# Performance work log

Hardware: AMD Instinct MI355X
Metric: run time of the kernel (lower is better)

The kernel has to match this reference:

```python
import jax, jax.numpy as jnp
import numpy as np
from jax import lax

DIM = 256
NUM_HEADS = 8
HEAD_DIM = DIM // NUM_HEADS  # 32
TOPK = 4
SCALE = 2  # spatial upscale factor between upper_feat grid and x grid


def conv1x1(x, W, b):
    # x: [B,Cin,H,W], W: [Cout,Cin], b: [Cout]
    return jnp.einsum('bchw,oc->bohw', x, W) + b[None, :, None, None]


def setup_inputs() -> dict:
    key = jax.random.key(0)
    ks = jax.random.split(key, 12)
    f32 = jnp.float32
    B, C, H, W = 2, DIM, 64, 64
    Hu, Wu = H // 2, W // 2
    s = 0.05
    return {
        'x': jax.random.normal(ks[0], (B, C, H, W), f32),
        'upper_feat': jax.random.normal(ks[1], (B, C, Hu, Wu), f32),
        # q: Conv(dim, all_head_dim, 1) with BN folded -> weight + bias
        'Wq': jax.random.normal(ks[2], (DIM, DIM), f32) * s,
        'bq': jnp.zeros((DIM,), f32),
        # kv: Conv(dim, 2*all_head_dim, 1)
        'Wkv': jax.random.normal(ks[3], (2 * DIM, DIM), f32) * s,
        'bkv': jnp.zeros((2 * DIM,), f32),
        # proj: Conv(all_head_dim, dim, 1)
        'Wproj': jax.random.normal(ks[4], (DIM, DIM), f32) * s,
        'bproj': jnp.zeros((DIM,), f32),
        # pe: depthwise 7x7 conv, groups=dim -> weight [dim,1,7,7]
        'Wpe': jax.random.normal(ks[5], (DIM, 1, 7, 7), f32) * s,
        'bpe': jnp.zeros((DIM,), f32),
        # gate_conv1d: Conv1d(2*head_dim, head_dim, 1) -> [head_dim, 2*head_dim]
        'Wg': jax.random.normal(ks[6], (HEAD_DIM, 2 * HEAD_DIM), f32) * s,
        'bg': jnp.zeros((HEAD_DIM,), f32),
    }


def reference(x, upper_feat, Wq, bq, Wkv, bkv, Wproj, bproj, Wpe, bpe, Wg, bg):
    B, C, H, W = x.shape
    N = H * W
    Hu, Wu = upper_feat.shape[2], upper_feat.shape[3]
    Nu = Hu * Wu
    nh, hd = NUM_HEADS, HEAD_DIM

    # queries from lower feature, keys/values from upper feature
    q = conv1x1(x, Wq, bq).reshape(B, nh, hd, N).transpose(0, 1, 3, 2)        # [B,h,N,hd]
    kv = conv1x1(upper_feat, Wkv, bkv).reshape(B, nh, 2 * hd, Nu).transpose(0, 1, 3, 2)
    k, v = kv[..., :hd], kv[..., hd:]                                         # [B,h,Nu,hd]

    sim = jnp.einsum('bhnd,bhmd->bhnm', q, k) * (hd ** -0.5)                  # [B,h,N,Nu]
    attn = jax.nn.softmax(sim, axis=-1)
    coarse_out = jnp.einsum('bhnm,bhmd->bhnd', attn, v)                       # [B,h,N,hd]

    # fine path: gumbel top-k selection over upper grid, gather 2x2 blocks from x grid
    f_kv = conv1x1(x, Wkv, bkv).reshape(B, nh, 2 * hd, N).transpose(0, 1, 3, 2)
    f_k, f_v = f_kv[..., :hd], f_kv[..., hd:]                                 # [B,h,N,hd]

    global_sim = sim.mean(axis=2)                                             # [B,h,Nu]
    gumbel = jax.random.gumbel(jax.random.key(42), global_sim.shape, global_sim.dtype)
    soft_weights = jax.nn.softmax(global_sim + gumbel, axis=-1)
    _, topk_idx = lax.top_k(soft_weights, TOPK)                               # [B,h,topk]

    h_idx = (topk_idx // Wu) * SCALE
    w_idx = (topk_idx % Wu) * SCALE
    idx = jnp.concatenate(
        [(h_idx + dh) * W + (w_idx + dw) for dh in range(SCALE) for dw in range(SCALE)],
        axis=-1,
    )                                                                          # [B,h,4*topk]

    topk_k = jnp.take_along_axis(f_k, idx[..., None], axis=2)                 # [B,h,4*topk,hd]
    topk_v = jnp.take_along_axis(f_v, idx[..., None], axis=2)

    fine_attn = jax.nn.softmax(jnp.einsum('bhnd,bhmd->bhnm', q, topk_k) * (hd ** -0.5), axis=-1)
    refined_out = jnp.einsum('bhnm,bhmd->bhnd', fine_attn, topk_v)            # [B,h,N,hd]

    fusion = jnp.concatenate([coarse_out, refined_out], axis=-1)              # [B,h,N,2hd]
    gate = jax.nn.sigmoid(jnp.einsum('bhnc,dc->bhnd', fusion, Wg) + bg)       # [B,h,N,hd]
    out = gate * refined_out + (1.0 - gate) * coarse_out

    out = out.transpose(0, 1, 3, 2).reshape(B, C, H, W)

    # positional encoding path: depthwise 7x7 conv on v, bilinear upsample
    v_r = v.transpose(0, 1, 3, 2).reshape(B, C, Hu, Wu)
    v_pe = lax.conv_general_dilated(
        v_r, Wpe, window_strides=(1, 1), padding=((3, 3), (3, 3)),
        dimension_numbers=('NCHW', 'OIHW', 'NCHW'), feature_group_count=C,
    ) + bpe[None, :, None, None]
    v_pe = jax.image.resize(v_pe, (B, C, H, W), method='bilinear')

    return conv1x1(out + v_pe, Wproj, bproj)
```

## Files before the change

### kernel.cpp

```cpp
#include <hip/hip_runtime.h>
#include <hip/hip_bf16.h>
#include <math.h>
#include <stdint.h>

#define NB   2
#define NC   256
#define NSP  4096
#define NUSP 1024
#define NHEADS 8
#define HDIM 32
constexpr float SCL  = 0.17677669529663687f;
constexpr float QSCL = 0.17677669529663687f * 1.4426950408889634f;

typedef short short8 __attribute__((ext_vector_type(8)));
typedef float f32x4  __attribute__((ext_vector_type(4)));

__device__ __forceinline__ float fexp2(float x) {
#if __has_builtin(__builtin_amdgcn_exp2f)
  return __builtin_amdgcn_exp2f(x);
#else
  return exp2f(x);
#endif
}

__device__ __align__(16) float g_kv    [NB * 512 * NUSP];
__device__ __align__(16) float g_qm    [NB * NHEADS * HDIM];
__device__ __align__(16) float g_vpe   [NB * NC * NSP];
__device__ __align__(16) short g_qbf   [NB * NHEADS * NSP * HDIM];
__device__ __align__(16) short g_kbf   [NB * NHEADS * NUSP * HDIM];
__device__ __align__(16) short g_vbf   [NB * NHEADS * HDIM * NUSP];
__device__ __align__(16) short g_tkKbf [NB * NHEADS * 16 * 32];
__device__ __align__(16) short g_tkVT  [NB * NHEADS * 32 * 32];
__device__ __align__(16) short g_xT    [NB * NSP * 256];
__device__ __align__(16) short g_uT    [NB * NUSP * 256];
__device__ __align__(16) short g_sumT  [NB * NSP * 256];
__device__ __align__(16) short g_wbf   [262144];
__device__ __align__(16) short g_wgbf  [2048];

__device__ __forceinline__ short f2bf(float f) {
  return (short)((__float_as_uint(f) + 0x8000u) >> 16);
}

__device__ __forceinline__ uint32_t pk2bf(float a, float b) {
  uint32_t lo = (__float_as_uint(a) + 0x8000u) >> 16;
  uint32_t hi = (__float_as_uint(b) + 0x8000u) & 0xffff0000u;
  return lo | hi;
}

__device__ __forceinline__ void threefry2x32_042(uint32_t x0, uint32_t x1,
                                                 uint32_t& r0, uint32_t& r1) {
  const uint32_t ks0 = 0u, ks1 = 42u, ks2 = 0u ^ 42u ^ 0x1BD11BDAu;
  x0 += ks0; x1 += ks1;
#define TFR(R) { x0 += x1; x1 = (x1 << (R)) | (x1 >> (32 - (R))); x1 ^= x0; }
  TFR(13) TFR(15) TFR(26) TFR(6)  x0 += ks1; x1 += ks2 + 1u;
  TFR(17) TFR(29) TFR(16) TFR(24) x0 += ks2; x1 += ks0 + 2u;
  TFR(13) TFR(15) TFR(26) TFR(6)  x0 += ks0; x1 += ks1 + 3u;
  TFR(17) TFR(29) TFR(16) TFR(24) x0 += ks1; x1 += ks2 + 4u;
  TFR(13) TFR(15) TFR(26) TFR(6)  x0 += ks2; x1 += ks0 + 5u;
#undef TFR
  r0 = x0; r1 = x1;
}

__device__ __forceinline__ float gumbel_at(uint32_t i) {
  uint32_t y0, y1;
  threefry2x32_042(0u, i, y0, y1);
  uint32_t bits = y0 ^ y1;
  uint32_t fb = (bits >> 9) | 0x3f800000u;
  float u = __uint_as_float(fb) - 1.0f;
  u = fmaxf(u, 1.17549435e-38f);
  return -logf(-logf(u));
}

__global__ __launch_bounds__(256) void k_pack_in(const float* __restrict__ x,
                                                 const float* __restrict__ upper,
                                                 const float* __restrict__ Wq,
                                                 const float* __restrict__ Wkv,
                                                 const float* __restrict__ Wproj,
                                                 const float* __restrict__ Wg) {
  const int sec = blockIdx.x;
  const int tid = threadIdx.x;
  if (sec < 160) {
    __shared__ float Ls[32][65];
    const float* src;
    short* dst;
    int b, n0, Nsp;
    if (sec < 128) { b = sec >> 6; n0 = (sec & 63) * 64; Nsp = NSP;
                     src = x + (size_t)b * 256 * NSP;  dst = g_xT + (size_t)b * NSP * 256; }
    else           { int s2 = sec - 128; b = s2 >> 4; n0 = (s2 & 15) * 64; Nsp = NUSP;
                     src = upper + (size_t)b * 256 * NUSP; dst = g_uT + (size_t)b * NUSP * 256; }
    for (int cc = 0; cc < 8; cc++) {
      __syncthreads();
      for (int i = tid; i < 2048; i += 256) {
        int d = i >> 6, nl = i & 63;
        Ls[d][nl] = src[(size_t)(cc * 32 + d) * Nsp + n0 + nl];
      }
      __syncthreads();
      int nl = tid >> 2, dseg = (tid & 3) * 8;
      short8 v;
      #pragma unroll
      for (int j = 0; j < 8; j++) v[j] = f2bf(Ls[dseg + j][nl]);
      *(short8*)&dst[(size_t)(n0 + nl) * 256 + cc * 32 + dseg] = v;
    }
  } else {
    if (sec == 160) {
      for (int i = tid; i < 512; i += 256) g_qm[i] = 0.f;
      #pragma unroll
      for (int j = 0; j < 8; j++) g_wgbf[tid * 8 + j] = f2bf(Wg[tid * 8 + j]);
    }
    int base = (sec - 160) * 8192 + tid * 32;
    const float* s;
    if (base < 65536)       s = Wq + base;
    else if (base < 196608) s = Wkv + (base - 65536);
    else                    s = Wproj + (base - 196608);
    short* d = g_wbf + base;
    #pragma unroll
    for (int j = 0; j < 8; j++) {
      float4 f = *(const float4*)&s[j * 4];
      d[j*4+0] = f2bf(f.x); d[j*4+1] = f2bf(f.y);
      d[j*4+2] = f2bf(f.z); d[j*4+3] = f2bf(f.w);
    }
  }
}

__device__ __forceinline__ void gemm_mfma(const short* __restrict__ Wbf,
                                          const short* __restrict__ ST,
                                          int b, int o0, int n0, int Nsp,
                                          int w, int col, int quad,
                                          f32x4 acc[4]) {
  const short* wrow = Wbf + (size_t)(o0 + w * 16 + col) * 256 + quad * 8;
  const short* srow = ST + ((size_t)b * Nsp + n0 + col) * 256 + quad * 8;
  #pragma unroll
  for (int kc = 0; kc < 8; kc++) {
    short8 af = *(const short8*)&wrow[kc * 32];
    #pragma unroll
    for (int t = 0; t < 4; t++) {
      short8 bf = *(const short8*)&srow[(size_t)(t * 16) * 256 + kc * 32];
      acc[t] = __builtin_amdgcn_mfma_f32_16x16x32_bf16(af, bf, acc[t], 0, 0, 0);
    }
  }
}

__global__ __launch_bounds__(256) void k_gemms(const float* __restrict__ bq,
                                               const float* __restrict__ bkv) {
  __shared__ float Ls[64][65];
  const int bx = blockIdx.x;
  const int tid = threadIdx.x;
  const int lane = tid & 63, w = tid >> 6, col = lane & 15, quad = lane >> 4;
  f32x4 acc[4] = {{0,0,0,0},{0,0,0,0},{0,0,0,0},{0,0,0,0}};

  if (bx < 512) {
    const int b = bx >> 8, o0 = ((bx >> 6) & 3) * 64, n0 = (bx & 63) * 64;
    gemm_mfma(g_wbf, g_xT, b, o0, n0, NSP, w, col, quad, acc);
    float sums[4];
    #pragma unroll
    for (int r = 0; r < 4; r++) {
      int ol = w * 16 + quad * 4 + r;
      float bv = bq[o0 + ol];
      float s = 0.f;
      #pragma unroll
      for (int t = 0; t < 4; t++) {
        float val = acc[t][r] + bv;
        Ls[ol][t * 16 + col] = val;
        s += val;
      }
      sums[r] = s;
    }
    #pragma unroll
    for (int st = 1; st < 16; st <<= 1)
      #pragma unroll
      for (int r = 0; r < 4; r++) sums[r] += __shfl_xor(sums[r], st, 64);
    if (col == 0) {
      #pragma unroll
      for (int r = 0; r < 4; r++)
        atomicAdd(&g_qm[b * 256 + o0 + w * 16 + quad * 4 + r], sums[r] * (1.0f / 4096.0f));
    }
    __syncthreads();
    int nl = tid >> 2, dseg = (tid & 3) * 8;
    #pragma unroll
    for (int hh = 0; hh < 2; hh++) {
      short8 v;
      #pragma unroll
      for (int j = 0; j < 8; j++) v[j] = f2bf(Ls[hh * 32 + dseg + j][nl] * QSCL);
      int bh = b * 8 + ((o0 + hh * 32) >> 5);
      *(short8*)&g_qbf[((size_t)bh * NSP + n0 + nl) * 32 + dseg] = v;
    }
  } else {
    const int idx = bx - 512;
    const int b = idx >> 7, o0 = ((idx >> 4) & 7) * 64, n0 = (idx & 15) * 64;
    gemm_mfma(g_wbf + 65536, g_uT, b, o0, n0, NUSP, w, col, quad, acc);
    #pragma unroll
    for (int r = 0; r < 4; r++) {
      int ol = w * 16 + quad * 4 + r;
      float bv = bkv[o0 + ol];
      float* orow = g_kv + ((size_t)b * 512 + o0 + ol) * NUSP + n0;
      #pragma unroll
      for (int t = 0; t < 4; t++) {
        float val = acc[t][r] + bv;
        orow[t * 16 + col] = val;
        Ls[ol][t * 16 + col] = val;
      }
    }
    __syncthreads();
    const int bh = b * 8 + (o0 >> 6);
    {
      int m = tid >> 2, dseg = (tid & 3) * 8;
      short8 v;
      #pragma unroll
      for (int j = 0; j < 8; j++) v[j] = f2bf(Ls[dseg + j][m]);
      *(short8*)&g_kbf[((size_t)bh * NUSP + n0 + m) * 32 + dseg] = v;
    }
    {
      int d = tid >> 3, m8 = (tid & 7) * 8;
      short8 v;
      #pragma unroll
      for (int j = 0; j < 8; j++) v[j] = f2bf(Ls[32 + d][m8 + j]);
      *(short8*)&g_vbf[((size_t)bh * 32 + d) * NUSP + n0 + m8] = v;
    }
  }
}

union MidSmem {
  struct {
    float zbuf[1024]; float qml[32]; float rv[256]; int ri[256];
    int chosen[4]; int pos[16]; float xg[16][256]; float wl[64][65];
  } t;
  struct {
    float src[32][33]; float pl[32][33]; float wk[49];
  } v;
};

__global__ __launch_bounds__(256) void k_mid(const float* __restrict__ x,
                                             const float* __restrict__ Wkv,
                                             const float* __restrict__ bkv,
                                             const float* __restrict__ Wpe,
                                             const float* __restrict__ bpe) {
  __shared__ MidSmem sm;
  const int tid = threadIdx.x;
  if (blockIdx.x < 16) {
    const int bh = blockIdx.x;
    const int b = bh >> 3, h = bh & 7;
    if (tid < 32) sm.t.qml[tid] = g_qm[bh * 32 + tid];
    __syncthreads();
    const float* kbase = g_kv + ((size_t)b * 512 + h * 64) * NUSP;
    float zv[4];
    #pragma unroll
    for (int r = 0; r < 4; r++) {
      int m = r * 256 + tid;
      float dot = 0.f;
      #pragma unroll 8
      for (int d = 0; d < 32; d++) dot += sm.t.qml[d] * kbase[(size_t)d * NUSP + m];
      float z = dot * SCL + gumbel_at((uint32_t)(bh * 1024 + m));
      zv[r] = z; sm.t.zbuf[m] = z;
    }
    __syncthreads();
    float mx = fmaxf(fmaxf(zv[0], zv[1]), fmaxf(zv[2], zv[3]));
    sm.t.rv[tid] = mx; __syncthreads();
    for (int st = 128; st > 0; st >>= 1) {
      if (tid < st) sm.t.rv[tid] = fmaxf(sm.t.rv[tid], sm.t.rv[tid + st]);
      __syncthreads();
    }
    float zmax = sm.t.rv[0]; __syncthreads();
    float sp = 0.f; float ev[4];
    #pragma unroll
    for (int r = 0; r < 4; r++) { ev[r] = __expf(zv[r] - zmax); sp += ev[r]; }
    sm.t.rv[tid] = sp; __syncthreads();
    for (int st = 128; st > 0; st >>= 1) {
      if (tid < st) sm.t.rv[tid] += sm.t.rv[tid + st];
      __syncthreads();
    }
    float ssum = sm.t.rv[0]; __syncthreads();
    #pragma unroll
    for (int r = 0; r < 4; r++) sm.t.zbuf[r * 256 + tid] = ev[r] / ssum;
    __syncthreads();
    for (int t = 0; t < 4; t++) {
      float bv = -2.0f; int bi = 0;
      #pragma unroll
      for (int r = 0; r < 4; r++) {
        int m = r * 256 + tid;
        float v = sm.t.zbuf[m];
        if (v > bv) { bv = v; bi = m; }
      }
      sm.t.rv[tid] = bv; sm.t.ri[tid] = bi; __syncthreads();
      for (int st = 128; st > 0; st >>= 1) {
        if (tid < st) {
          float v2 = sm.t.rv[tid + st]; int i2 = sm.t.ri[tid + st];
          if (v2 > sm.t.rv[tid] || (v2 == sm.t.rv[tid] && i2 < sm.t.ri[tid])) {
            sm.t.rv[tid] = v2; sm.t.ri[tid] = i2;
          }
        }
        __syncthreads();
      }
      if (tid == 0) { sm.t.chosen[t] = sm.t.ri[0]; sm.t.zbuf[sm.t.ri[0]] = -2.0f; }
      __syncthreads();
    }
    if (tid < 16) {
      int t = tid & 3, g2 = tid >> 2;
      int dh = g2 >> 1, dw = g2 & 1;
      int m = sm.t.chosen[t];
      int hi = (m >> 5) * 2 + dh, wi = (m & 31) * 2 + dw;
      sm.t.pos[g2 * 4 + t] = hi * 64 + wi;
    }
    __syncthreads();
    for (int i = tid; i < 16 * 256; i += 256) {
      int j = i >> 8, c = i & 255;
      sm.t.xg[j][c] = x[((size_t)b * 256 + c) * NSP + sm.t.pos[j]];
    }
    const int dd = tid & 63, jg = tid >> 6;
    const float bia = bkv[h * 64 + dd];
    float a4[4] = {bia, bia, bia, bia};
    for (int cc2 = 0; cc2 < 4; cc2++) {
      __syncthreads();
      for (int i = tid; i < 4096; i += 256) {
        int r = i >> 6, c = i & 63;
        sm.t.wl[r][c] = Wkv[(size_t)(h * 64 + r) * 256 + cc2 * 64 + c];
      }
      __syncthreads();
      #pragma unroll
      for (int jj = 0; jj < 4; jj++) {
        int j = jg * 4 + jj;
        float a = 0.f;
        #pragma unroll 8
        for (int c = 0; c < 64; c++) a += sm.t.xg[j][cc2 * 64 + c] * sm.t.wl[dd][c];
        a4[jj] += a;
      }
    }
    #pragma unroll
    for (int jj = 0; jj < 4; jj++) {
      int j = jg * 4 + jj;
      if (dd < 32) {
        g_tkKbf[((size_t)bh * 16 + j) * 32 + dd] = f2bf(a4[jj]);
      } else {
        int d = dd - 32;
        g_tkVT[((size_t)bh * 32 + d) * 32 + j] = f2bf(a4[jj]);
        g_tkVT[((size_t)bh * 32 + d) * 32 + 16 + j] = 0;
      }
    }
  } else {
    const int idx = blockIdx.x - 16;
    const int c = idx & 255, b = idx >> 8;
    const int h = c >> 5, d = c & 31;
    const float* vrow = g_kv + ((size_t)b * 512 + h * 64 + 32 + d) * NUSP;
    for (int i = tid; i < 1024; i += 256) sm.v.src[i >> 5][i & 31] = vrow[i];
    if (tid < 49) sm.v.wk[tid] = Wpe[c * 49 + tid];
    __syncthreads();
    const float bia = bpe[c];
    for (int i = tid; i < 1024; i += 256) {
      int hu = i >> 5, wu = i & 31;
      float s = bia;
      #pragma unroll
      for (int kh = 0; kh < 7; kh++) {
        int ih = hu + kh - 3;
        if (ih < 0 || ih > 31) continue;
        #pragma unroll
        for (int kw = 0; kw < 7; kw++) {
          int iw = wu + kw - 3;
          if (iw < 0 || iw > 31) continue;
          s += sm.v.src[ih][iw] * sm.v.wk[kh * 7 + kw];
        }
      }
      sm.v.pl[hu][wu] = s;
    }
    __syncthreads();
    float* orow = g_vpe + ((size_t)b * 256 + c) * NSP;
    for (int i = tid; i < 4096; i += 256) {
      int hh = i >> 6, ww = i & 63;
      int ih = hh >> 1, iw = ww >> 1;
      int ih2 = (hh & 1) ? min(ih + 1, 31) : max(ih - 1, 0);
      int iw2 = (ww & 1) ? min(iw + 1, 31) : max(iw - 1, 0);
      float a  = 0.75f * sm.v.pl[ih][iw]  + 0.25f * sm.v.pl[ih][iw2];
      float bb = 0.75f * sm.v.pl[ih2][iw] + 0.25f * sm.v.pl[ih2][iw2];
      orow[i] = 0.75f * a + 0.25f * bb;
    }
  }
}

__global__ __launch_bounds__(256) void k_flash(const float* __restrict__ bg) {
  const int bh = blockIdx.y;
  const int b = bh >> 3, h = bh & 7;
  const int tid = threadIdx.x;
  const int lane = tid & 63;
  const int w = tid >> 6;
  const int col = lane & 15;
  const int quad = lane >> 4;
  const int n0 = blockIdx.x * 128 + w * 32;

  __shared__ __align__(16) short Ps[8][16][88];
  short* PsA = &Ps[w * 2][0][0];
  short* PsB = &Ps[w * 2 + 1][0][0];

  const short* kb = g_kbf + (size_t)bh * NUSP * 32;
  const short* vb = g_vbf + (size_t)bh * 32 * NUSP;

  short8 qfA = *(const short8*)&g_qbf[((size_t)bh * NSP + n0 + col) * 32 + quad * 8];
  short8 qfB = *(const short8*)&g_qbf[((size_t)bh * NSP + n0 + 16 + col) * 32 + quad * 8];

  f32x4 oA0 = {0,0,0,0}, oA1 = {0,0,0,0}, oB0 = {0,0,0,0}, oB1 = {0,0,0,0};
  float lA = 0.f, lB = 0.f;

  for (int kt = 0; kt < 16; kt++) {
    short8 kf[4];
    #pragma unroll
    for (int t = 0; t < 4; t++)
      kf[t] = *(const short8*)&kb[((size_t)(kt * 64 + t * 16 + col)) * 32 + quad * 8];
    f32x4 sA[4], sB[4];
    #pragma unroll
    for (int t = 0; t < 4; t++) {
      f32x4 z = {0,0,0,0};
      sA[t] = __builtin_amdgcn_mfma_f32_16x16x32_bf16(kf[t], qfA, z, 0, 0, 0);
      sB[t] = __builtin_amdgcn_mfma_f32_16x16x32_bf16(kf[t], qfB, z, 0, 0, 0);
    }
    #pragma unroll
    for (int t = 0; t < 4; t++) {
      float a0 = fexp2(sA[t][0]), a1 = fexp2(sA[t][1]);
      float a2 = fexp2(sA[t][2]), a3 = fexp2(sA[t][3]);
      lA += (a0 + a1) + (a2 + a3);
      uint2 wa; wa.x = pk2bf(a0, a1); wa.y = pk2bf(a2, a3);
      *(uint2*)&PsA[col * 88 + t * 16 + quad * 4] = wa;
      float b0 = fexp2(sB[t][0]), b1 = fexp2(sB[t][1]);
      float b2 = fexp2(sB[t][2]), b3 = fexp2(sB[t][3]);
      lB += (b0 + b1) + (b2 + b3);
      uint2 wb; wb.x = pk2bf(b0, b1); wb.y = pk2bf(b2, b3);
      *(uint2*)&PsB[col * 88 + t * 16 + quad * 4] = wb;
    }
    short8 vf0 = *(const short8*)&vb[(size_t)col * NUSP + kt * 64 + quad * 8];
    short8 vf1 = *(const short8*)&vb[(size_t)(col + 16) * NUSP + kt * 64 + quad * 8];
    short8 vf2 = *(const short8*)&vb[(size_t)col * NUSP + kt * 64 + 32 + quad * 8];
    short8 vf3 = *(const short8*)&vb[(size_t)(col + 16) * NUSP + kt * 64 + 32 + quad * 8];
    short8 pA0 = *(const short8*)&PsA[col * 88 + quad * 8];
    short8 pA1 = *(const short8*)&PsA[col * 88 + 32 + quad * 8];
    short8 pB0 = *(const short8*)&PsB[col * 88 + quad * 8];
    short8 pB1 = *(const short8*)&PsB[col * 88 + 32 + quad * 8];
    oA0 = __builtin_amdgcn_mfma_f32_16x16x32_bf16(pA0, vf0, oA0, 0, 0, 0);
    oB0 = __builtin_amdgcn_mfma_f32_16x16x32_bf16(pB0, vf0, oB0, 0, 0, 0);
    oA1 = __builtin_amdgcn_mfma_f32_16x16x32_bf16(pA0, vf1, oA1, 0, 0, 0);
    oB1 = __builtin_amdgcn_mfma_f32_16x16x32_bf16(pB0, vf1, oB1, 0, 0, 0);
    oA0 = __builtin_amdgcn_mfma_f32_16x16x32_bf16(pA1, vf2, oA0, 0, 0, 0);
    oB0 = __builtin_amdgcn_mfma_f32_16x16x32_bf16(pB1, vf2, oB0, 0, 0, 0);
    oA1 = __builtin_amdgcn_mfma_f32_16x16x32_bf16(pA1, vf3, oA1, 0, 0, 0);
    oB1 = __builtin_amdgcn_mfma_f32_16x16x32_bf16(pB1, vf3, oB1, 0, 0, 0);
  }
  lA += __shfl_xor(lA, 16, 64); lA += __shfl_xor(lA, 32, 64);
  lB += __shfl_xor(lB, 16, 64); lB += __shfl_xor(lB, 32, 64);

  const float bg0 = bg[col], bg1 = bg[col + 16];
  short8 kff = *(const short8*)&g_tkKbf[(size_t)bh * 512 + col * 32 + quad * 8];
  short8 vt0 = *(const short8*)&g_tkVT[(size_t)bh * 1024 + col * 32 + quad * 8];
  short8 vt1 = *(const short8*)&g_tkVT[(size_t)bh * 1024 + (col + 16) * 32 + quad * 8];
  short8 b1a = *(const short8*)&g_wgbf[col * 64 + quad * 8];
  short8 b1b = *(const short8*)&g_wgbf[col * 64 + 32 + quad * 8];
  short8 b2a = *(const short8*)&g_wgbf[(col + 16) * 64 + quad * 8];
  short8 b2b = *(const short8*)&g_wgbf[(col + 16) * 64 + 32 + quad * 8];

  #pragma unroll
  for (int tt = 0; tt < 2; tt++) {
    const int nt = n0 + tt * 16;
    short8 qf = tt ? qfB : qfA;
    f32x4 o0 = tt ? oB0 : oA0;
    f32x4 o1 = tt ? oB1 : oA1;
    float lt = tt ? lB : lA;
    short* myPs = tt ? PsB : PsA;
    f32x4 zf = {0,0,0,0};
    f32x4 co0, co1;
    #pragma unroll
    for (int r = 0; r < 4; r++) {
      float inv = 1.0f / __shfl(lt, quad * 4 + r, 64);
      co0[r] = o0[r] * inv;
      co1[r] = o1[r] * inv;
    }
    f32x4 sfT = __builtin_amdgcn_mfma_f32_16x16x32_bf16(kff, qf, zf, 0, 0, 0);
    float p0 = fexp2(sfT[0]), p1 = fexp2(sfT[1]);
    float p2 = fexp2(sfT[2]), p3 = fexp2(sfT[3]);
    float fls = (p0 + p1) + (p2 + p3);
    uint2 wf; wf.x = pk2bf(p0, p1); wf.y = pk2bf(p2, p3);
    *(uint2*)&myPs[col * 88 + quad * 4] = wf;
    fls += __shfl_xor(fls, 16, 64);
    fls += __shfl_xor(fls, 32, 64);
    short8 pff = {0, 0, 0, 0, 0, 0, 0, 0};
    if (quad < 2) pff = *(const short8*)&myPs[col * 88 + quad * 8];
    f32x4 rf0 = __builtin_amdgcn_mfma_f32_16x16x32_bf16(pff, vt0, zf, 0, 0, 0);
    f32x4 rf1 = __builtin_amdgcn_mfma_f32_16x16x32_bf16(pff, vt1, zf, 0, 0, 0);
    #pragma unroll
    for (int r = 0; r < 4; r++) {
      float inv = 1.0f / __shfl(fls, quad * 4 + r, 64);
      rf0[r] *= inv; rf1[r] *= inv;
    }
    #pragma unroll
    for (int r = 0; r < 4; r++) {
      int q = quad * 4 + r;
      myPs[q * 88 + col]      = f2bf(co0[r]);
      myPs[q * 88 + col + 16] = f2bf(co1[r]);
      myPs[q * 88 + col + 32] = f2bf(rf0[r]);
      myPs[q * 88 + col + 48] = f2bf(rf1[r]);
    }
    short8 a1 = *(const short8*)&myPs[col * 88 + quad * 8];
    short8 a2 = *(const short8*)&myPs[col * 88 + 32 + quad * 8];
    f32x4 G0 = __builtin_amdgcn_mfma_f32_16x16x32_bf16(a1, b1a, zf, 0, 0, 0);
    G0 = __builtin_amdgcn_mfma_f32_16x16x32_bf16(a2, b1b, G0, 0, 0, 0);
    f32x4 G1 = __builtin_amdgcn_mfma_f32_16x16x32_bf16(a1, b2a, zf, 0, 0, 0);
    G1 = __builtin_amdgcn_mfma_f32_16x16x32_bf16(a2, b2b, G1, 0, 0, 0);
    const float* vpe0 = g_vpe + ((size_t)(b * 256 + h * 32 + col)) * NSP + nt;
    const float* vpe1 = g_vpe + ((size_t)(b * 256 + h * 32 + col + 16)) * NSP + nt;
    short* dstb = g_sumT + ((size_t)b * NSP + nt) * 256 + h * 32;
    #pragma unroll
    for (int r = 0; r < 4; r++) {
      int q = quad * 4 + r;
      float g0 = 1.0f / (1.0f + __expf(-(G0[r] + bg0)));
      float g1 = 1.0f / (1.0f + __expf(-(G1[r] + bg1)));
      float out0 = g0 * rf0[r] + (1.0f - g0) * co0[r] + vpe0[q];
      float out1 = g1 * rf1[r] + (1.0f - g1) * co1[r] + vpe1[q];
      dstb[(size_t)q * 256 + col]      = f2bf(out0);
      dstb[(size_t)q * 256 + col + 16] = f2bf(out1);
    }
  }
}

__global__ __launch_bounds__(256) void k_gemm_proj(const float* __restrict__ bias,
                                                   float* __restrict__ out) {
  const int b = blockIdx.z;
  const int o0 = blockIdx.y * 64;
  const int n0 = blockIdx.x * 64;
  const int tid = threadIdx.x;
  const int lane = tid & 63, w = tid >> 6, col = lane & 15, quad = lane >> 4;
  f32x4 acc[4] = {{0,0,0,0},{0,0,0,0},{0,0,0,0},{0,0,0,0}};
  gemm_mfma(g_wbf + 196608, g_sumT, b, o0, n0, NSP, w, col, quad, acc);
  #pragma unroll
  for (int r = 0; r < 4; r++) {
    int o = o0 + w * 16 + quad * 4 + r;
    float bv = bias[o];
    float* orow = out + ((size_t)b * 256 + o) * NSP + n0;
    #pragma unroll
    for (int t = 0; t < 4; t++)
      orow[t * 16 + col] = acc[t][r] + bv;
  }
}

extern "C" void kernel_launch(void* const* d_in, const int* in_sizes, int n_in,
                              void* d_out, int out_size, void* d_ws, size_t ws_size,
                              hipStream_t stream) {
  const float* x     = (const float*)d_in[0];
  const float* upper = (const float*)d_in[1];
  const float* Wq    = (const float*)d_in[2];
  const float* bq    = (const float*)d_in[3];
  const float* Wkv   = (const float*)d_in[4];
  const float* bkv   = (const float*)d_in[5];
  const float* Wproj = (const float*)d_in[6];
  const float* bproj = (const float*)d_in[7];
  const float* Wpe   = (const float*)d_in[8];
  const float* bpe   = (const float*)d_in[9];
  const float* Wg    = (const float*)d_in[10];
  const float* bg    = (const float*)d_in[11];
  float* out = (float*)d_out;
  (void)d_ws; (void)ws_size; (void)in_sizes; (void)n_in; (void)out_size;

  k_pack_in<<<dim3(192), dim3(256), 0, stream>>>(x, upper, Wq, Wkv, Wproj, Wg);
  k_gemms<<<dim3(768), dim3(256), 0, stream>>>(bq, bkv);
  k_mid<<<dim3(528), dim3(256), 0, stream>>>(x, Wkv, bkv, Wpe, bpe);
  k_flash<<<dim3(32, 16), dim3(256), 0, stream>>>(bg);
  k_gemm_proj<<<dim3(64, 4, 2), dim3(256), 0, stream>>>(bproj, out);
}
```

Baseline: 204.9 us.

## Fuse five kernels into one persistent kernel with software grid barriers

Merges the pack, projection GEMMs, mid (top-k and positional conv), flash attention and output projection kernels into one persistent kernel of 512 blocks. Stages are separated by atomic-counter grid barriers instead of kernel launches, and each stage loops over its original block indices. The aim is to remove launch overhead and the idle gaps between dependent kernels. In exchange, all blocks must be co-resident to avoid deadlock, so occupancy is limited by the shared-memory union and launch bounds, and a stage with fewer work items leaves blocks waiting at the barrier.

```diff
diff --git a/kernel.cpp b/kernel.cpp
--- a/kernel.cpp
+++ b/kernel.cpp
@@ -9,6 +9,7 @@
 #define NUSP 1024
 #define NHEADS 8
 #define HDIM 32
+#define NBLK 512
 constexpr float SCL  = 0.17677669529663687f;
 constexpr float QSCL = 0.17677669529663687f * 1.4426950408889634f;
 
@@ -37,6 +38,23 @@
 __device__ __align__(16) short g_wbf   [262144];
 __device__ __align__(16) short g_wgbf  [2048];
 
+__device__ unsigned g_barrier[8];
+
+__device__ __forceinline__ void grid_barrier(int idx) {
+  __syncthreads();
+  if (threadIdx.x == 0) {
+    __threadfence();
+    unsigned v = __hip_atomic_fetch_add(&g_barrier[idx], 1u,
+                                        __ATOMIC_RELEASE, __HIP_MEMORY_SCOPE_AGENT);
+    unsigned target = (v / NBLK + 1u) * (unsigned)NBLK;
+    while (__hip_atomic_load(&g_barrier[idx], __ATOMIC_ACQUIRE,
+                             __HIP_MEMORY_SCOPE_AGENT) < target)
+      __builtin_amdgcn_s_sleep(2);
+    __threadfence();
+  }
+  __syncthreads();
+}
+
 __device__ __forceinline__ short f2bf(float f) {
   return (short)((__float_as_uint(f) + 0x8000u) >> 16);
 }
@@ -69,57 +87,6 @@
   float u = __uint_as_float(fb) - 1.0f;
   u = fmaxf(u, 1.17549435e-38f);
   return -logf(-logf(u));
-}
-
-__global__ __launch_bounds__(256) void k_pack_in(const float* __restrict__ x,
-                                                 const float* __restrict__ upper,
-                                                 const float* __restrict__ Wq,
-                                                 const float* __restrict__ Wkv,
-                                                 const float* __restrict__ Wproj,
-                                                 const float* __restrict__ Wg) {
-  const int sec = blockIdx.x;
-  const int tid = threadIdx.x;
-  if (sec < 160) {
-    __shared__ float Ls[32][65];
-    const float* src;
-    short* dst;
-    int b, n0, Nsp;
-    if (sec < 128) { b = sec >> 6; n0 = (sec & 63) * 64; Nsp = NSP;
-                     src = x + (size_t)b * 256 * NSP;  dst = g_xT + (size_t)b * NSP * 256; }
-    else           { int s2 = sec - 128; b = s2 >> 4; n0 = (s2 & 15) * 64; Nsp = NUSP;
-                     src = upper + (size_t)b * 256 * NUSP; dst = g_uT + (size_t)b * NUSP * 256; }
-    for (int cc = 0; cc < 8; cc++) {
-      __syncthreads();
-      for (int i = tid; i < 2048; i += 256) {
-        int d = i >> 6, nl = i & 63;
-        Ls[d][nl] = src[(size_t)(cc * 32 + d) * Nsp + n0 + nl];
-      }
-      __syncthreads();
-      int nl = tid >> 2, dseg = (tid & 3) * 8;
-      short8 v;
-      #pragma unroll
-      for (int j = 0; j < 8; j++) v[j] = f2bf(Ls[dseg + j][nl]);
-      *(short8*)&dst[(size_t)(n0 + nl) * 256 + cc * 32 + dseg] = v;
-    }
-  } else {
-    if (sec == 160) {
-      for (int i = tid; i < 512; i += 256) g_qm[i] = 0.f;
-      #pragma unroll
-      for (int j = 0; j < 8; j++) g_wgbf[tid * 8 + j] = f2bf(Wg[tid * 8 + j]);
-    }
-    int base = (sec - 160) * 8192 + tid * 32;
-    const float* s;
-    if (base < 65536)       s = Wq + base;
-    else if (base < 196608) s = Wkv + (base - 65536);
-    else                    s = Wproj + (base - 196608);
-    short* d = g_wbf + base;
-    #pragma unroll
-    for (int j = 0; j < 8; j++) {
-      float4 f = *(const float4*)&s[j * 4];
-      d[j*4+0] = f2bf(f.x); d[j*4+1] = f2bf(f.y);
-      d[j*4+2] = f2bf(f.z); d[j*4+3] = f2bf(f.w);
-    }
-  }
 }
 
 __device__ __forceinline__ void gemm_mfma(const short* __restrict__ Wbf,
@@ -140,86 +107,7 @@
   }
 }
 
-__global__ __launch_bounds__(256) void k_gemms(const float* __restrict__ bq,
-                                               const float* __restrict__ bkv) {
-  __shared__ float Ls[64][65];
-  const int bx = blockIdx.x;
-  const int tid = threadIdx.x;
-  const int lane = tid & 63, w = tid >> 6, col = lane & 15, quad = lane >> 4;
-  f32x4 acc[4] = {{0,0,0,0},{0,0,0,0},{0,0,0,0},{0,0,0,0}};
-
-  if (bx < 512) {
-    const int b = bx >> 8, o0 = ((bx >> 6) & 3) * 64, n0 = (bx & 63) * 64;
-    gemm_mfma(g_wbf, g_xT, b, o0, n0, NSP, w, col, quad, acc);
-    float sums[4];
-    #pragma unroll
-    for (int r = 0; r < 4; r++) {
-      int ol = w * 16 + quad * 4 + r;
-      float bv = bq[o0 + ol];
-      float s = 0.f;
-      #pragma unroll
-      for (int t = 0; t < 4; t++) {
-        float val = acc[t][r] + bv;
-        Ls[ol][t * 16 + col] = val;
-        s += val;
-      }
-      sums[r] = s;
-    }
-    #pragma unroll
-    for (int st = 1; st < 16; st <<= 1)
-      #pragma unroll
-      for (int r = 0; r < 4; r++) sums[r] += __shfl_xor(sums[r], st, 64);
-    if (col == 0) {
-      #pragma unroll
-      for (int r = 0; r < 4; r++)
-        atomicAdd(&g_qm[b * 256 + o0 + w * 16 + quad * 4 + r], sums[r] * (1.0f / 4096.0f));
-    }
-    __syncthreads();
-    int nl = tid >> 2, dseg = (tid & 3) * 8;
-    #pragma unroll
-    for (int hh = 0; hh < 2; hh++) {
-      short8 v;
-      #pragma unroll
-      for (int j = 0; j < 8; j++) v[j] = f2bf(Ls[hh * 32 + dseg + j][nl] * QSCL);
-      int bh = b * 8 + ((o0 + hh * 32) >> 5);
-      *(short8*)&g_qbf[((size_t)bh * NSP + n0 + nl) * 32 + dseg] = v;
-    }
-  } else {
-    const int idx = bx - 512;
-    const int b = idx >> 7, o0 = ((idx >> 4) & 7) * 64, n0 = (idx & 15) * 64;
-    gemm_mfma(g_wbf + 65536, g_uT, b, o0, n0, NUSP, w, col, quad, acc);
-    #pragma unroll
-    for (int r = 0; r < 4; r++) {
-      int ol = w * 16 + quad * 4 + r;
-      float bv = bkv[o0 + ol];
-      float* orow = g_kv + ((size_t)b * 512 + o0 + ol) * NUSP + n0;
-      #pragma unroll
-      for (int t = 0; t < 4; t++) {
-        float val = acc[t][r] + bv;
-        orow[t * 16 + col] = val;
-        Ls[ol][t * 16 + col] = val;
-      }
-    }
-    __syncthreads();
-    const int bh = b * 8 + (o0 >> 6);
-    {
-      int m = tid >> 2, dseg = (tid & 3) * 8;
-      short8 v;
-      #pragma unroll
-      for (int j = 0; j < 8; j++) v[j] = f2bf(Ls[dseg + j][m]);
-      *(short8*)&g_kbf[((size_t)bh * NUSP + n0 + m) * 32 + dseg] = v;
-    }
-    {
-      int d = tid >> 3, m8 = (tid & 7) * 8;
-      short8 v;
-      #pragma unroll
-      for (int j = 0; j < 8; j++) v[j] = f2bf(Ls[32 + d][m8 + j]);
-      *(short8*)&g_vbf[((size_t)bh * 32 + d) * NUSP + n0 + m8] = v;
-    }
-  }
-}
-
-union MidSmem {
+union __align__(16) FusedSmem {
   struct {
     float zbuf[1024]; float qml[32]; float rv[256]; int ri[256];
     int chosen[4]; int pos[16]; float xg[16][256]; float wl[64][65];
@@ -227,310 +115,440 @@
   struct {
     float src[32][33]; float pl[32][33]; float wk[49];
   } v;
+  float gls[64][65];
+  short Ps[8][16][88];
 };
 
-__global__ __launch_bounds__(256) void k_mid(const float* __restrict__ x,
-                                             const float* __restrict__ Wkv,
-                                             const float* __restrict__ bkv,
-                                             const float* __restrict__ Wpe,
-                                             const float* __restrict__ bpe) {
-  __shared__ MidSmem sm;
+__global__ __launch_bounds__(256, 2) void k_fused(const float* __restrict__ x,
+                                                  const float* __restrict__ upper,
+                                                  const float* __restrict__ Wq,
+                                                  const float* __restrict__ bq,
+                                                  const float* __restrict__ Wkv,
+                                                  const float* __restrict__ bkv,
+                                                  const float* __restrict__ Wproj,
+                                                  const float* __restrict__ bproj,
+                                                  const float* __restrict__ Wpe,
+                                                  const float* __restrict__ bpe,
+                                                  const float* __restrict__ Wg,
+                                                  const float* __restrict__ bg,
+                                                  float* __restrict__ out) {
+  __shared__ FusedSmem sm;
+  const int blk = blockIdx.x;
   const int tid = threadIdx.x;
-  if (blockIdx.x < 16) {
-    const int bh = blockIdx.x;
+  const int lane = tid & 63, w = tid >> 6, col = lane & 15, quad = lane >> 4;
+
+  if (blk < 192) {
+    const int sec = blk;
+    if (sec < 160) {
+      const float* src;
+      short* dst;
+      int b, n0, Nsp;
+      if (sec < 128) { b = sec >> 6; n0 = (sec & 63) * 64; Nsp = NSP;
+                       src = x + (size_t)b * 256 * NSP;  dst = g_xT + (size_t)b * NSP * 256; }
+      else           { int s2 = sec - 128; b = s2 >> 4; n0 = (s2 & 15) * 64; Nsp = NUSP;
+                       src = upper + (size_t)b * 256 * NUSP; dst = g_uT + (size_t)b * NUSP * 256; }
+      for (int cc = 0; cc < 8; cc++) {
+        __syncthreads();
+        for (int i = tid; i < 2048; i += 256) {
+          int d = i >> 6, nl = i & 63;
+          sm.gls[d][nl] = src[(size_t)(cc * 32 + d) * Nsp + n0 + nl];
+        }
+        __syncthreads();
+        int nl = tid >> 2, dseg = (tid & 3) * 8;
+        short8 vv;
+        #pragma unroll
+        for (int j = 0; j < 8; j++) vv[j] = f2bf(sm.gls[dseg + j][nl]);
+        *(short8*)&dst[(size_t)(n0 + nl) * 256 + cc * 32 + dseg] = vv;
+      }
+    } else {
+      if (sec == 160) {
+        for (int i = tid; i < 512; i += 256) g_qm[i] = 0.f;
+        #pragma unroll
+        for (int j = 0; j < 8; j++) g_wgbf[tid * 8 + j] = f2bf(Wg[tid * 8 + j]);
+      }
+      int base = (sec - 160) * 8192 + tid * 32;
+      const float* s;
+      if (base < 65536)       s = Wq + base;
+      else if (base < 196608) s = Wkv + (base - 65536);
+      else                    s = Wproj + (base - 196608);
+      short* d = g_wbf + base;
+      #pragma unroll
+      for (int j = 0; j < 8; j++) {
+        float4 f = *(const float4*)&s[j * 4];
+        d[j*4+0] = f2bf(f.x); d[j*4+1] = f2bf(f.y);
+        d[j*4+2] = f2bf(f.z); d[j*4+3] = f2bf(f.w);
+      }
+    }
+  }
+  grid_barrier(0);
+
+  for (int bx = blk; bx < 768; bx += NBLK) {
+    __syncthreads();
+    f32x4 acc[4] = {{0,0,0,0},{0,0,0,0},{0,0,0,0},{0,0,0,0}};
+    if (bx < 512) {
+      const int b = bx >> 8, o0 = ((bx >> 6) & 3) * 64, n0 = (bx & 63) * 64;
+      gemm_mfma(g_wbf, g_xT, b, o0, n0, NSP, w, col, quad, acc);
+      float sums[4];
+      #pragma unroll
+      for (int r = 0; r < 4; r++) {
+        int ol = w * 16 + quad * 4 + r;
+        float bv = bq[o0 + ol];
+        float s = 0.f;
+        #pragma unroll
+        for (int t = 0; t < 4; t++) {
+          float val = acc[t][r] + bv;
+          sm.gls[ol][t * 16 + col] = val;
+          s += val;
+        }
+        sums[r] = s;
+      }
+      #pragma unroll
+      for (int st = 1; st < 16; st <<= 1)
+        #pragma unroll
+        for (int r = 0; r < 4; r++) sums[r] += __shfl_xor(sums[r], st, 64);
+      if (col == 0) {
+        #pragma unroll
+        for (int r = 0; r < 4; r++)
+          atomicAdd(&g_qm[b * 256 + o0 + w * 16 + quad * 4 + r], sums[r] * (1.0f / 4096.0f));
+      }
+      __syncthreads();
+      int nl = tid >> 2, dseg = (tid & 3) * 8;
+      #pragma unroll
+      for (int hh = 0; hh < 2; hh++) {
+        short8 vv;
+        #pragma unroll
+        for (int j = 0; j < 8; j++) vv[j] = f2bf(sm.gls[hh * 32 + dseg + j][nl] * QSCL);
+        int bh = b * 8 + ((o0 + hh * 32) >> 5);
+        *(short8*)&g_qbf[((size_t)bh * NSP + n0 + nl) * 32 + dseg] = vv;
+      }
+    } else {
+      const int idx = bx - 512;
+      const int b = idx >> 7, o0 = ((idx >> 4) & 7) * 64, n0 = (idx & 15) * 64;
+      gemm_mfma(g_wbf + 65536, g_uT, b, o0, n0, NUSP, w, col, quad, acc);
+      #pragma unroll
+      for (int r = 0; r < 4; r++) {
+        int ol = w * 16 + quad * 4 + r;
+        float bv = bkv[o0 + ol];
+        float* orow = g_kv + ((size_t)b * 512 + o0 + ol) * NUSP + n0;
+        #pragma unroll
+        for (int t = 0; t < 4; t++) {
+          float val = acc[t][r] + bv;
+          orow[t * 16 + col] = val;
+          sm.gls[ol][t * 16 + col] = val;
+        }
+      }
+      __syncthreads();
+      const int bh = b * 8 + (o0 >> 6);
+      {
+        int m = tid >> 2, dseg = (tid & 3) * 8;
+        short8 vv;
+        #pragma unroll
+        for (int j = 0; j < 8; j++) vv[j] = f2bf(sm.gls[dseg + j][m]);
+        *(short8*)&g_kbf[((size_t)bh * NUSP + n0 + m) * 32 + dseg] = vv;
+      }
+      {
+        int d = tid >> 3, m8 = (tid & 7) * 8;
+        short8 vv;
+        #pragma unroll
+        for (int j = 0; j < 8; j++) vv[j] = f2bf(sm.gls[32 + d][m8 + j]);
+        *(short8*)&g_vbf[((size_t)bh * 32 + d) * NUSP + n0 + m8] = vv;
+      }
+    }
+  }
+  grid_barrier(1);
+
+  for (int t528 = blk; t528 < 528; t528 += NBLK) {
+    __syncthreads();
+    if (t528 < 16) {
+      const int bh = t528;
+      const int b = bh >> 3, h = bh & 7;
+      if (tid < 32) sm.t.qml[tid] = g_qm[bh * 32 + tid];
+      __syncthreads();
+      const float* kbase = g_kv + ((size_t)b * 512 + h * 64) * NUSP;
+      float zv[4];
+      #pragma unroll
+      for (int r = 0; r < 4; r++) {
+        int m = r * 256 + tid;
+        float dot = 0.f;
+        #pragma unroll 8
+        for (int d = 0; d < 32; d++) dot += sm.t.qml[d] * kbase[(size_t)d * NUSP + m];
+        float z = dot * SCL + gumbel_at((uint32_t)(bh * 1024 + m));
+        zv[r] = z; sm.t.zbuf[m] = z;
+      }
+      __syncthreads();
+      float mx = fmaxf(fmaxf(zv[0], zv[1]), fmaxf(zv[2], zv[3]));
+      sm.t.rv[tid] = mx; __syncthreads();
+      for (int st = 128; st > 0; st >>= 1) {
+        if (tid < st) sm.t.rv[tid] = fmaxf(sm.t.rv[tid], sm.t.rv[tid + st]);
+        __syncthreads();
+      }
+      float zmax = sm.t.rv[0]; __syncthreads();
+      float sp = 0.f; float ev[4];
+      #pragma unroll
+      for (int r = 0; r < 4; r++) { ev[r] = __expf(zv[r] - zmax); sp += ev[r]; }
+      sm.t.rv[tid] = sp; __syncthreads();
+      for (int st = 128; st > 0; st >>= 1) {
+        if (tid < st) sm.t.rv[tid] += sm.t.rv[tid + st];
+        __syncthreads();
+      }
+      float ssum = sm.t.rv[0]; __syncthreads();
+      #pragma unroll
+      for (int r = 0; r < 4; r++) sm.t.zbuf[r * 256 + tid] = ev[r] / ssum;
+      __syncthreads();
+      for (int t = 0; t < 4; t++) {
+        float bv = -2.0f; int bi = 0;
+        #pragma unroll
+        for (int r = 0; r < 4; r++) {
+          int m = r * 256 + tid;
+          float v = sm.t.zbuf[m];
+          if (v > bv) { bv = v; bi = m; }
+        }
+        sm.t.rv[tid] = bv; sm.t.ri[tid] = bi; __syncthreads();
+        for (int st = 128; st > 0; st >>= 1) {
+          if (tid < st) {
+            float v2 = sm.t.rv[tid + st]; int i2 = sm.t.ri[tid + st];
+            if (v2 > sm.t.rv[tid] || (v2 == sm.t.rv[tid] && i2 < sm.t.ri[tid])) {
+              sm.t.rv[tid] = v2; sm.t.ri[tid] = i2;
+            }
+          }
+          __syncthreads();
+        }
+        if (tid == 0) { sm.t.chosen[t] = sm.t.ri[0]; sm.t.zbuf[sm.t.ri[0]] = -2.0f; }
+        __syncthreads();
+      }
+      if (tid < 16) {
+        int t = tid & 3, g2 = tid >> 2;
+        int dh = g2 >> 1, dw = g2 & 1;
+        int m = sm.t.chosen[t];
+        int hi = (m >> 5) * 2 + dh, wi = (m & 31) * 2 + dw;
+        sm.t.pos[g2 * 4 + t] = hi * 64 + wi;
+      }
+      __syncthreads();
+      for (int i = tid; i < 16 * 256; i += 256) {
+        int j = i >> 8, c = i & 255;
+        sm.t.xg[j][c] = x[((size_t)b * 256 + c) * NSP + sm.t.pos[j]];
+      }
+      const int dd = tid & 63, jg = tid >> 6;
+      const float bia = bkv[h * 64 + dd];
+      float a4[4] = {bia, bia, bia, bia};
+      for (int cc2 = 0; cc2 < 4; cc2++) {
+        __syncthreads();
+        for (int i = tid; i < 4096; i += 256) {
+          int r = i >> 6, c = i & 63;
+          sm.t.wl[r][c] = Wkv[(size_t)(h * 64 + r) * 256 + cc2 * 64 + c];
+        }
+        __syncthreads();
+        #pragma unroll
+        for (int jj = 0; jj < 4; jj++) {
+          int j = jg * 4 + jj;
+          float a = 0.f;
+          #pragma unroll 8
+          for (int c = 0; c < 64; c++) a += sm.t.xg[j][cc2 * 64 + c] * sm.t.wl[dd][c];
+          a4[jj] += a;
+        }
+      }
+      #pragma unroll
+      for (int jj = 0; jj < 4; jj++) {
+        int j = jg * 4 + jj;
+        if (dd < 32) {
+          g_tkKbf[((size_t)bh * 16 + j) * 32 + dd] = f2bf(a4[jj]);
+        } else {
+          int d = dd - 32;
+          g_tkVT[((size_t)bh * 32 + d) * 32 + j] = f2bf(a4[jj]);
+          g_tkVT[((size_t)bh * 32 + d) * 32 + 16 + j] = 0;
+        }
+      }
+    } else {
+      const int idx = t528 - 16;
+      const int c = idx & 255, b = idx >> 8;
+      const int h = c >> 5, d = c & 31;
+      const float* vrow = g_kv + ((size_t)b * 512 + h * 64 + 32 + d) * NUSP;
+      for (int i = tid; i < 1024; i += 256) sm.v.src[i >> 5][i & 31] = vrow[i];
+      if (tid < 49) sm.v.wk[tid] = Wpe[c * 49 + tid];
+      __syncthreads();
+      const float bia = bpe[c];
+      for (int i = tid; i < 1024; i += 256) {
+        int hu = i >> 5, wu = i & 31;
+        float s = bia;
+        #pragma unroll
+        for (int kh = 0; kh < 7; kh++) {
+          int ih = hu + kh - 3;
+          if (ih < 0 || ih > 31) continue;
+          #pragma unroll
+          for (int kw = 0; kw < 7; kw++) {
+            int iw = wu + kw - 3;
+            if (iw < 0 || iw > 31) continue;
+            s += sm.v.src[ih][iw] * sm.v.wk[kh * 7 + kw];
+          }
+        }
+        sm.v.pl[hu][wu] = s;
+      }
+      __syncthreads();
+      float* orow = g_vpe + ((size_t)b * 256 + c) * NSP;
+      for (int i = tid; i < 4096; i += 256) {
+        int hh = i >> 6, ww = i & 63;
+        int ih = hh >> 1, iw = ww >> 1;
+        int ih2 = (hh & 1) ? min(ih + 1, 31) : max(ih - 1, 0);
+        int iw2 = (ww & 1) ? min(iw + 1, 31) : max(iw - 1, 0);
+        float a  = 0.75f * sm.v.pl[ih][iw]  + 0.25f * sm.v.pl[ih][iw2];
+        float bb = 0.75f * sm.v.pl[ih2][iw] + 0.25f * sm.v.pl[ih2][iw2];
+        orow[i] = 0.75f * a + 0.25f * bb;
+      }
+    }
+  }
+  grid_barrier(2);
+
+  {
+    const int bxf = blk & 31;
+    const int bh  = blk >> 5;
     const int b = bh >> 3, h = bh & 7;
-    if (tid < 32) sm.t.qml[tid] = g_qm[bh * 32 + tid];
-    __syncthreads();
-    const float* kbase = g_kv + ((size_t)b * 512 + h * 64) * NUSP;
-    float zv[4];
+    const int n0 = bxf * 128 + w * 32;
+
+    short* PsA = &sm.Ps[w * 2][0][0];
+    short* PsB = &sm.Ps[w * 2 + 1][0][0];
+
+    const short* kb = g_kbf + (size_t)bh * NUSP * 32;
+    const short* vb = g_vbf + (size_t)bh * 32 * NUSP;
+
+    short8 qfA = *(const short8*)&g_qbf[((size_t)bh * NSP + n0 + col) * 32 + quad * 8];
+    short8 qfB = *(const short8*)&g_qbf[((size_t)bh * NSP + n0 + 16 + col) * 32 + quad * 8];
+
+    f32x4 oA0 = {0,0,0,0}, oA1 = {0,0,0,0}, oB0 = {0,0,0,0}, oB1 = {0,0,0,0};
+    float lA = 0.f, lB = 0.f;
+
+    for (int kt = 0; kt < 16; kt++) {
+      short8 kf[4];
+      #pragma unroll
+      for (int t = 0; t < 4; t++)
+        kf[t] = *(const short8*)&kb[((size_t)(kt * 64 + t * 16 + col)) * 32 + quad * 8];
+      f32x4 sA[4], sB[4];
+      #pragma unroll
+      for (int t = 0; t < 4; t++) {
+        f32x4 z = {0,0,0,0};
+        sA[t] = __builtin_amdgcn_mfma_f32_16x16x32_bf16(kf[t], qfA, z, 0, 0, 0);
+        sB[t] = __builtin_amdgcn_mfma_f32_16x16x32_bf16(kf[t], qfB, z, 0, 0, 0);
+      }
+      #pragma unroll
+      for (int t = 0; t < 4; t++) {
+        float a0 = fexp2(sA[t][0]), a1 = fexp2(sA[t][1]);
+        float a2 = fexp2(sA[t][2]), a3 = fexp2(sA[t][3]);
+        lA += (a0 + a1) + (a2 + a3);
+        uint2 wa; wa.x = pk2bf(a0, a1); wa.y = pk2bf(a2, a3);
+        *(uint2*)&PsA[col * 88 + t * 16 + quad * 4] = wa;
+        float b0 = fexp2(sB[t][0]), b1 = fexp2(sB[t][1]);
+        float b2 = fexp2(sB[t][2]), b3 = fexp2(sB[t][3]);
+        lB += (b0 + b1) + (b2 + b3);
+        uint2 wb; wb.x = pk2bf(b0, b1); wb.y = pk2bf(b2, b3);
+        *(uint2*)&PsB[col * 88 + t * 16 + quad * 4] = wb;
+      }
+      short8 vf0 = *(const short8*)&vb[(size_t)col * NUSP + kt * 64 + quad * 8];
+      short8 vf1 = *(const short8*)&vb[(size_t)(col + 16) * NUSP + kt * 64 + quad * 8];
+      short8 vf2 = *(const short8*)&vb[(size_t)col * NUSP + kt * 64 + 32 + quad * 8];
+      short8 vf3 = *(const short8*)&vb[(size_t)(col + 16) * NUSP + kt * 64 + 32 + quad * 8];
+      short8 pA0 = *(const short8*)&PsA[col * 88 + quad * 8];
+      short8 pA1 = *(const short8*)&PsA[col * 88 + 32 + quad * 8];
+      short8 pB0 = *(const short8*)&PsB[col * 88 + quad * 8];
+      short8 pB1 = *(const short8*)&PsB[col * 88 + 32 + quad * 8];
+      oA0 = __builtin_amdgcn_mfma_f32_16x16x32_bf16(pA0, vf0, oA0, 0, 0, 0);
+      oB0 = __builtin_amdgcn_mfma_f32_16x16x32_bf16(pB0, vf0, oB0, 0, 0, 0);
+      oA1 = __builtin_amdgcn_mfma_f32_16x16x32_bf16(pA0, vf1, oA1, 0, 0, 0);
+      oB1 = __builtin_amdgcn_mfma_f32_16x16x32_bf16(pB0, vf1, oB1, 0, 0, 0);
+      oA0 = __builtin_amdgcn_mfma_f32_16x16x32_bf16(pA1, vf2, oA0, 0, 0, 0);
+      oB0 = __builtin_amdgcn_mfma_f32_16x16x32_bf16(pB1, vf2, oB0, 0, 0, 0);
+      oA1 = __builtin_amdgcn_mfma_f32_16x16x32_bf16(pA1, vf3, oA1, 0, 0, 0);
+      oB1 = __builtin_amdgcn_mfma_f32_16x16x32_bf16(pB1, vf3, oB1, 0, 0, 0);
+    }
+    lA += __shfl_xor(lA, 16, 64); lA += __shfl_xor(lA, 32, 64);
+    lB += __shfl_xor(lB, 16, 64); lB += __shfl_xor(lB, 32, 64);
+
+    const float bg0 = bg[col], bg1 = bg[col + 16];
+    short8 kff = *(const short8*)&g_tkKbf[(size_t)bh * 512 + col * 32 + quad * 8];
+    short8 vt0 = *(const short8*)&g_tkVT[(size_t)bh * 1024 + col * 32 + quad * 8];
+    short8 vt1 = *(const short8*)&g_tkVT[(size_t)bh * 1024 + (col + 16) * 32 + quad * 8];
+    short8 b1a = *(const short8*)&g_wgbf[col * 64 + quad * 8];
+    short8 b1b = *(const short8*)&g_wgbf[col * 64 + 32 + quad * 8];
+    short8 b2a = *(const short8*)&g_wgbf[(col + 16) * 64 + quad * 8];
+    short8 b2b = *(const short8*)&g_wgbf[(col + 16) * 64 + 32 + quad * 8];
+
+    #pragma unroll
+    for (int tt = 0; tt < 2; tt++) {
+      const int nt = n0 + tt * 16;
+      short8 qf = tt ? qfB : qfA;
+      f32x4 o0 = tt ? oB0 : oA0;
+      f32x4 o1 = tt ? oB1 : oA1;
+      float lt = tt ? lB : lA;
+      short* myPs = tt ? PsB : PsA;
+      f32x4 zf = {0,0,0,0};
+      f32x4 co0, co1;
+      #pragma unroll
+      for (int r = 0; r < 4; r++) {
+        float inv = 1.0f / __shfl(lt, quad * 4 + r, 64);
+        co0[r] = o0[r] * inv;
+        co1[r] = o1[r] * inv;
+      }
+      f32x4 sfT = __builtin_amdgcn_mfma_f32_16x16x32_bf16(kff, qf, zf, 0, 0, 0);
+      float p0 = fexp2(sfT[0]), p1 = fexp2(sfT[1]);
+      float p2 = fexp2(sfT[2]), p3 = fexp2(sfT[3]);
+      float fls = (p0 + p1) + (p2 + p3);
+      uint2 wf; wf.x = pk2bf(p0, p1); wf.y = pk2bf(p2, p3);
+      *(uint2*)&myPs[col * 88 + quad * 4] = wf;
+      fls += __shfl_xor(fls, 16, 64);
+      fls += __shfl_xor(fls, 32, 64);
+      short8 pff = {0, 0, 0, 0, 0, 0, 0, 0};
+      if (quad < 2) pff = *(const short8*)&myPs[col * 88 + quad * 8];
+      f32x4 rf0 = __builtin_amdgcn_mfma_f32_16x16x32_bf16(pff, vt0, zf, 0, 0, 0);
+      f32x4 rf1 = __builtin_amdgcn_mfma_f32_16x16x32_bf16(pff, vt1, zf, 0, 0, 0);
+      #pragma unroll
+      for (int r = 0; r < 4; r++) {
+        float inv = 1.0f / __shfl(fls, quad * 4 + r, 64);
+        rf0[r] *= inv; rf1[r] *= inv;
+      }
+      #pragma unroll
+      for (int r = 0; r < 4; r++) {
+        int q = quad * 4 + r;
+        myPs[q * 88 + col]      = f2bf(co0[r]);
+        myPs[q * 88 + col + 16] = f2bf(co1[r]);
+        myPs[q * 88 + col + 32] = f2bf(rf0[r]);
+        myPs[q * 88 + col + 48] = f2bf(rf1[r]);
+      }
+      short8 a1 = *(const short8*)&myPs[col * 88 + quad * 8];
+      short8 a2 = *(const short8*)&myPs[col * 88 + 32 + quad * 8];
+      f32x4 G0 = __builtin_amdgcn_mfma_f32_16x16x32_bf16(a1, b1a, zf, 0, 0, 0);
+      G0 = __builtin_amdgcn_mfma_f32_16x16x32_bf16(a2, b1b, G0, 0, 0, 0);
+      f32x4 G1 = __builtin_amdgcn_mfma_f32_16x16x32_bf16(a1, b2a, zf, 0, 0, 0);
+      G1 = __builtin_amdgcn_mfma_f32_16x16x32_bf16(a2, b2b, G1, 0, 0, 0);
+      const float* vpe0 = g_vpe + ((size_t)(b * 256 + h * 32 + col)) * NSP + nt;
+      const float* vpe1 = g_vpe + ((size_t)(b * 256 + h * 32 + col + 16)) * NSP + nt;
+      short* dstb = g_sumT + ((size_t)b * NSP + nt) * 256 + h * 32;
+      #pragma unroll
+      for (int r = 0; r < 4; r++) {
+        int q = quad * 4 + r;
+        float g0 = 1.0f / (1.0f + __expf(-(G0[r] + bg0)));
+        float g1 = 1.0f / (1.0f + __expf(-(G1[r] + bg1)));
+        float out0 = g0 * rf0[r] + (1.0f - g0) * co0[r] + vpe0[q];
+        float out1 = g1 * rf1[r] + (1.0f - g1) * co1[r] + vpe1[q];
+        dstb[(size_t)q * 256 + col]      = f2bf(out0);
+        dstb[(size_t)q * 256 + col + 16] = f2bf(out1);
+      }
+    }
+  }
+  grid_barrier(3);
+
+  {
+    const int b  = blk >> 8;
+    const int o0 = ((blk >> 6) & 3) * 64;
+    const int n0 = (blk & 63) * 64;
+    f32x4 acc[4] = {{0,0,0,0},{0,0,0,0},{0,0,0,0},{0,0,0,0}};
+    gemm_mfma(g_wbf + 196608, g_sumT, b, o0, n0, NSP, w, col, quad, acc);
     #pragma unroll
     for (int r = 0; r < 4; r++) {
-      int m = r * 256 + tid;
-      float dot = 0.f;
-      #pragma unroll 8
-      for (int d = 0; d < 32; d++) dot += sm.t.qml[d] * kbase[(size_t)d * NUSP + m];
-      float z = dot * SCL + gumbel_at((uint32_t)(bh * 1024 + m));
-      zv[r] = z; sm.t.zbuf[m] = z;
-    }
-    __syncthreads();
-    float mx = fmaxf(fmaxf(zv[0], zv[1]), fmaxf(zv[2], zv[3]));
-    sm.t.rv[tid] = mx; __syncthreads();
-    for (int st = 128; st > 0; st >>= 1) {
-      if (tid < st) sm.t.rv[tid] = fmaxf(sm.t.rv[tid], sm.t.rv[tid + st]);
-      __syncthreads();
-    }
-    float zmax = sm.t.rv[0]; __syncthreads();
-    float sp = 0.f; float ev[4];
-    #pragma unroll
-    for (int r = 0; r < 4; r++) { ev[r] = __expf(zv[r] - zmax); sp += ev[r]; }
-    sm.t.rv[tid] = sp; __syncthreads();
-    for (int st = 128; st > 0; st >>= 1) {
-      if (tid < st) sm.t.rv[tid] += sm.t.rv[tid + st];
-      __syncthreads();
-    }
-    float ssum = sm.t.rv[0]; __syncthreads();
-    #pragma unroll
-    for (int r = 0; r < 4; r++) sm.t.zbuf[r * 256 + tid] = ev[r] / ssum;
-    __syncthreads();
-    for (int t = 0; t < 4; t++) {
-      float bv = -2.0f; int bi = 0;
-      #pragma unroll
-      for (int r = 0; r < 4; r++) {
-        int m = r * 256 + tid;
-        float v = sm.t.zbuf[m];
-        if (v > bv) { bv = v; bi = m; }
-      }
-      sm.t.rv[tid] = bv; sm.t.ri[tid] = bi; __syncthreads();
-      for (int st = 128; st > 0; st >>= 1) {
-        if (tid < st) {
-          float v2 = sm.t.rv[tid + st]; int i2 = sm.t.ri[tid + st];
-          if (v2 > sm.t.rv[tid] || (v2 == sm.t.rv[tid] && i2 < sm.t.ri[tid])) {
-            sm.t.rv[tid] = v2; sm.t.ri[tid] = i2;
-          }
-        }
-        __syncthreads();
-      }
-      if (tid == 0) { sm.t.chosen[t] = sm.t.ri[0]; sm.t.zbuf[sm.t.ri[0]] = -2.0f; }
-      __syncthreads();
-    }
-    if (tid < 16) {
-      int t = tid & 3, g2 = tid >> 2;
-      int dh = g2 >> 1, dw = g2 & 1;
-      int m = sm.t.chosen[t];
-      int hi = (m >> 5) * 2 + dh, wi = (m & 31) * 2 + dw;
-      sm.t.pos[g2 * 4 + t] = hi * 64 + wi;
-    }
-    __syncthreads();
-    for (int i = tid; i < 16 * 256; i += 256) {
-      int j = i >> 8, c = i & 255;
-      sm.t.xg[j][c] = x[((size_t)b * 256 + c) * NSP + sm.t.pos[j]];
-    }
-    const int dd = tid & 63, jg = tid >> 6;
-    const float bia = bkv[h * 64 + dd];
-    float a4[4] = {bia, bia, bia, bia};
-    for (int cc2 = 0; cc2 < 4; cc2++) {
-      __syncthreads();
-      for (int i = tid; i < 4096; i += 256) {
-        int r = i >> 6, c = i & 63;
-        sm.t.wl[r][c] = Wkv[(size_t)(h * 64 + r) * 256 + cc2 * 64 + c];
-      }
-      __syncthreads();
-      #pragma unroll
-      for (int jj = 0; jj < 4; jj++) {
-        int j = jg * 4 + jj;
-        float a = 0.f;
-        #pragma unroll 8
-        for (int c = 0; c < 64; c++) a += sm.t.xg[j][cc2 * 64 + c] * sm.t.wl[dd][c];
-        a4[jj] += a;
-      }
-    }
-    #pragma unroll
-    for (int jj = 0; jj < 4; jj++) {
-      int j = jg * 4 + jj;
-      if (dd < 32) {
-        g_tkKbf[((size_t)bh * 16 + j) * 32 + dd] = f2bf(a4[jj]);
-      } else {
-        int d = dd - 32;
-        g_tkVT[((size_t)bh * 32 + d) * 32 + j] = f2bf(a4[jj]);
-        g_tkVT[((size_t)bh * 32 + d) * 32 + 16 + j] = 0;
-      }
-    }
-  } else {
-    const int idx = blockIdx.x - 16;
-    const int c = idx & 255, b = idx >> 8;
-    const int h = c >> 5, d = c & 31;
-    const float* vrow = g_kv + ((size_t)b * 512 + h * 64 + 32 + d) * NUSP;
-    for (int i = tid; i < 1024; i += 256) sm.v.src[i >> 5][i & 31] = vrow[i];
-    if (tid < 49) sm.v.wk[tid] = Wpe[c * 49 + tid];
-    __syncthreads();
-    const float bia = bpe[c];
-    for (int i = tid; i < 1024; i += 256) {
-      int hu = i >> 5, wu = i & 31;
-      float s = bia;
-      #pragma unroll
-      for (int kh = 0; kh < 7; kh++) {
-        int ih = hu + kh - 3;
-        if (ih < 0 || ih > 31) continue;
-        #pragma unroll
-        for (int kw = 0; kw < 7; kw++) {
-          int iw = wu + kw - 3;
-          if (iw < 0 || iw > 31) continue;
-          s += sm.v.src[ih][iw] * sm.v.wk[kh * 7 + kw];
-        }
-      }
-      sm.v.pl[hu][wu] = s;
-    }
-    __syncthreads();
-    float* orow = g_vpe + ((size_t)b * 256 + c) * NSP;
-    for (int i = tid; i < 4096; i += 256) {
-      int hh = i >> 6, ww = i & 63;
-      int ih = hh >> 1, iw = ww >> 1;
-      int ih2 = (hh & 1) ? min(ih + 1, 31) : max(ih - 1, 0);
-      int iw2 = (ww & 1) ? min(iw + 1, 31) : max(iw - 1, 0);
-      float a  = 0.75f * sm.v.pl[ih][iw]  + 0.25f * sm.v.pl[ih][iw2];
-      float bb = 0.75f * sm.v.pl[ih2][iw] + 0.25f * sm.v.pl[ih2][iw2];
-      orow[i] = 0.75f * a + 0.25f * bb;
-    }
-  }
-}
-
-__global__ __launch_bounds__(256) void k_flash(const float* __restrict__ bg) {
-  const int bh = blockIdx.y;
-  const int b = bh >> 3, h = bh & 7;
-  const int tid = threadIdx.x;
-  const int lane = tid & 63;
-  const int w = tid >> 6;
-  const int col = lane & 15;
-  const int quad = lane >> 4;
-  const int n0 = blockIdx.x * 128 + w * 32;
-
-  __shared__ __align__(16) short Ps[8][16][88];
-  short* PsA = &Ps[w * 2][0][0];
-  short* PsB = &Ps[w * 2 + 1][0][0];
-
-  const short* kb = g_kbf + (size_t)bh * NUSP * 32;
-  const short* vb = g_vbf + (size_t)bh * 32 * NUSP;
-
-  short8 qfA = *(const short8*)&g_qbf[((size_t)bh * NSP + n0 + col) * 32 + quad * 8];
-  short8 qfB = *(const short8*)&g_qbf[((size_t)bh * NSP + n0 + 16 + col) * 32 + quad * 8];
-
-  f32x4 oA0 = {0,0,0,0}, oA1 = {0,0,0,0}, oB0 = {0,0,0,0}, oB1 = {0,0,0,0};
-  float lA = 0.f, lB = 0.f;
-
-  for (int kt = 0; kt < 16; kt++) {
-    short8 kf[4];
-    #pragma unroll
-    for (int t = 0; t < 4; t++)
-      kf[t] = *(const short8*)&kb[((size_t)(kt * 64 + t * 16 + col)) * 32 + quad * 8];
-    f32x4 sA[4], sB[4];
-    #pragma unroll
-    for (int t = 0; t < 4; t++) {
-      f32x4 z = {0,0,0,0};
-      sA[t] = __builtin_amdgcn_mfma_f32_16x16x32_bf16(kf[t], qfA, z, 0, 0, 0);
-      sB[t] = __builtin_amdgcn_mfma_f32_16x16x32_bf16(kf[t], qfB, z, 0, 0, 0);
-    }
-    #pragma unroll
-    for (int t = 0; t < 4; t++) {
-      float a0 = fexp2(sA[t][0]), a1 = fexp2(sA[t][1]);
-      float a2 = fexp2(sA[t][2]), a3 = fexp2(sA[t][3]);
-      lA += (a0 + a1) + (a2 + a3);
-      uint2 wa; wa.x = pk2bf(a0, a1); wa.y = pk2bf(a2, a3);
-      *(uint2*)&PsA[col * 88 + t * 16 + quad * 4] = wa;
-      float b0 = fexp2(sB[t][0]), b1 = fexp2(sB[t][1]);
-      float b2 = fexp2(sB[t][2]), b3 = fexp2(sB[t][3]);
-      lB += (b0 + b1) + (b2 + b3);
-      uint2 wb; wb.x = pk2bf(b0, b1); wb.y = pk2bf(b2, b3);
-      *(uint2*)&PsB[col * 88 + t * 16 + quad * 4] = wb;
-    }
-    short8 vf0 = *(const short8*)&vb[(size_t)col * NUSP + kt * 64 + quad * 8];
-    short8 vf1 = *(const short8*)&vb[(size_t)(col + 16) * NUSP + kt * 64 + quad * 8];
-    short8 vf2 = *(const short8*)&vb[(size_t)col * NUSP + kt * 64 + 32 + quad * 8];
-    short8 vf3 = *(const short8*)&vb[(size_t)(col + 16) * NUSP + kt * 64 + 32 + quad * 8];
-    short8 pA0 = *(const short8*)&PsA[col * 88 + quad * 8];
-    short8 pA1 = *(const short8*)&PsA[col * 88 + 32 + quad * 8];
-    short8 pB0 = *(const short8*)&PsB[col * 88 + quad * 8];
-    short8 pB1 = *(const short8*)&PsB[col * 88 + 32 + quad * 8];
-    oA0 = __builtin_amdgcn_mfma_f32_16x16x32_bf16(pA0, vf0, oA0, 0, 0, 0);
-    oB0 = __builtin_amdgcn_mfma_f32_16x16x32_bf16(pB0, vf0, oB0, 0, 0, 0);
-    oA1 = __builtin_amdgcn_mfma_f32_16x16x32_bf16(pA0, vf1, oA1, 0, 0, 0);
-    oB1 = __builtin_amdgcn_mfma_f32_16x16x32_bf16(pB0, vf1, oB1, 0, 0, 0);
-    oA0 = __builtin_amdgcn_mfma_f32_16x16x32_bf16(pA1, vf2, oA0, 0, 0, 0);
-    oB0 = __builtin_amdgcn_mfma_f32_16x16x32_bf16(pB1, vf2, oB0, 0, 0, 0);
-    oA1 = __builtin_amdgcn_mfma_f32_16x16x32_bf16(pA1, vf3, oA1, 0, 0, 0);
-    oB1 = __builtin_amdgcn_mfma_f32_16x16x32_bf16(pB1, vf3, oB1, 0, 0, 0);
-  }
-  lA += __shfl_xor(lA, 16, 64); lA += __shfl_xor(lA, 32, 64);
-  lB += __shfl_xor(lB, 16, 64); lB += __shfl_xor(lB, 32, 64);
-
-  const float bg0 = bg[col], bg1 = bg[col + 16];
-  short8 kff = *(const short8*)&g_tkKbf[(size_t)bh * 512 + col * 32 + quad * 8];
-  short8 vt0 = *(const short8*)&g_tkVT[(size_t)bh * 1024 + col * 32 + quad * 8];
-  short8 vt1 = *(const short8*)&g_tkVT[(size_t)bh * 1024 + (col + 16) * 32 + quad * 8];
-  short8 b1a = *(const short8*)&g_wgbf[col * 64 + quad * 8];
-  short8 b1b = *(const short8*)&g_wgbf[col * 64 + 32 + quad * 8];
-  short8 b2a = *(const short8*)&g_wgbf[(col + 16) * 64 + quad * 8];
-  short8 b2b = *(const short8*)&g_wgbf[(col + 16) * 64 + 32 + quad * 8];
-
-  #pragma unroll
-  for (int tt = 0; tt < 2; tt++) {
-    const int nt = n0 + tt * 16;
-    short8 qf = tt ? qfB : qfA;
-    f32x4 o0 = tt ? oB0 : oA0;
-    f32x4 o1 = tt ? oB1 : oA1;
-    float lt = tt ? lB : lA;
-    short* myPs = tt ? PsB : PsA;
-    f32x4 zf = {0,0,0,0};
-    f32x4 co0, co1;
-    #pragma unroll
-    for (int r = 0; r < 4; r++) {
-      float inv = 1.0f / __shfl(lt, quad * 4 + r, 64);
-      co0[r] = o0[r] * inv;
-      co1[r] = o1[r] * inv;
-    }
-    f32x4 sfT = __builtin_amdgcn_mfma_f32_16x16x32_bf16(kff, qf, zf, 0, 0, 0);
-    float p0 = fexp2(sfT[0]), p1 = fexp2(sfT[1]);
-    float p2 = fexp2(sfT[2]), p3 = fexp2(sfT[3]);
-    float fls = (p0 + p1) + (p2 + p3);
-    uint2 wf; wf.x = pk2bf(p0, p1); wf.y = pk2bf(p2, p3);
-    *(uint2*)&myPs[col * 88 + quad * 4] = wf;
-    fls += __shfl_xor(fls, 16, 64);
-    fls += __shfl_xor(fls, 32, 64);
-    short8 pff = {0, 0, 0, 0, 0, 0, 0, 0};
-    if (quad < 2) pff = *(const short8*)&myPs[col * 88 + quad * 8];
-    f32x4 rf0 = __builtin_amdgcn_mfma_f32_16x16x32_bf16(pff, vt0, zf, 0, 0, 0);
-    f32x4 rf1 = __builtin_amdgcn_mfma_f32_16x16x32_bf16(pff, vt1, zf, 0, 0, 0);
-    #pragma unroll
-    for (int r = 0; r < 4; r++) {
-      float inv = 1.0f / __shfl(fls, quad * 4 + r, 64);
-      rf0[r] *= inv; rf1[r] *= inv;
-    }
-    #pragma unroll
-    for (int r = 0; r < 4; r++) {
-      int q = quad * 4 + r;
-      myPs[q * 88 + col]      = f2bf(co0[r]);
-      myPs[q * 88 + col + 16] = f2bf(co1[r]);
-      myPs[q * 88 + col + 32] = f2bf(rf0[r]);
-      myPs[q * 88 + col + 48] = f2bf(rf1[r]);
-    }
-    short8 a1 = *(const short8*)&myPs[col * 88 + quad * 8];
-    short8 a2 = *(const short8*)&myPs[col * 88 + 32 + quad * 8];
-    f32x4 G0 = __builtin_amdgcn_mfma_f32_16x16x32_bf16(a1, b1a, zf, 0, 0, 0);
-    G0 = __builtin_amdgcn_mfma_f32_16x16x32_bf16(a2, b1b, G0, 0, 0, 0);
-    f32x4 G1 = __builtin_amdgcn_mfma_f32_16x16x32_bf16(a1, b2a, zf, 0, 0, 0);
-    G1 = __builtin_amdgcn_mfma_f32_16x16x32_bf16(a2, b2b, G1, 0, 0, 0);
-    const float* vpe0 = g_vpe + ((size_t)(b * 256 + h * 32 + col)) * NSP + nt;
-    const float* vpe1 = g_vpe + ((size_t)(b * 256 + h * 32 + col + 16)) * NSP + nt;
-    short* dstb = g_sumT + ((size_t)b * NSP + nt) * 256 + h * 32;
-    #pragma unroll
-    for (int r = 0; r < 4; r++) {
-      int q = quad * 4 + r;
-      float g0 = 1.0f / (1.0f + __expf(-(G0[r] + bg0)));
-      float g1 = 1.0f / (1.0f + __expf(-(G1[r] + bg1)));
-      float out0 = g0 * rf0[r] + (1.0f - g0) * co0[r] + vpe0[q];
-      float out1 = g1 * rf1[r] + (1.0f - g1) * co1[r] + vpe1[q];
-      dstb[(size_t)q * 256 + col]      = f2bf(out0);
-      dstb[(size_t)q * 256 + col + 16] = f2bf(out1);
-    }
-  }
-}
-
-__global__ __launch_bounds__(256) void k_gemm_proj(const float* __restrict__ bias,
-                                                   float* __restrict__ out) {
-  const int b = blockIdx.z;
-  const int o0 = blockIdx.y * 64;
-  const int n0 = blockIdx.x * 64;
-  const int tid = threadIdx.x;
-  const int lane = tid & 63, w = tid >> 6, col = lane & 15, quad = lane >> 4;
-  f32x4 acc[4] = {{0,0,0,0},{0,0,0,0},{0,0,0,0},{0,0,0,0}};
-  gemm_mfma(g_wbf + 196608, g_sumT, b, o0, n0, NSP, w, col, quad, acc);
-  #pragma unroll
-  for (int r = 0; r < 4; r++) {
-    int o = o0 + w * 16 + quad * 4 + r;
-    float bv = bias[o];
-    float* orow = out + ((size_t)b * 256 + o) * NSP + n0;
-    #pragma unroll
-    for (int t = 0; t < 4; t++)
-      orow[t * 16 + col] = acc[t][r] + bv;
+      int o = o0 + w * 16 + quad * 4 + r;
+      float bv = bproj[o];
+      float* orow = out + ((size_t)b * 256 + o) * NSP + n0;
+      #pragma unroll
+      for (int t = 0; t < 4; t++)
+        orow[t * 16 + col] = acc[t][r] + bv;
+    }
   }
 }
 
@@ -552,9 +570,6 @@
   float* out = (float*)d_out;
   (void)d_ws; (void)ws_size; (void)in_sizes; (void)n_in; (void)out_size;
 
-  k_pack_in<<<dim3(192), dim3(256), 0, stream>>>(x, upper, Wq, Wkv, Wproj, Wg);
-  k_gemms<<<dim3(768), dim3(256), 0, stream>>>(bq, bkv);
-  k_mid<<<dim3(528), dim3(256), 0, stream>>>(x, Wkv, bkv, Wpe, bpe);
-  k_flash<<<dim3(32, 16), dim3(256), 0, stream>>>(bg);
-  k_gemm_proj<<<dim3(64, 4, 2), dim3(256), 0, stream>>>(bproj, out);
-}
+  k_fused<<<dim3(NBLK), dim3(256), 0, stream>>>(x, upper, Wq, bq, Wkv, bkv,
+                                                Wproj, bproj, Wpe, bpe, Wg, bg, out);
+}
```

Result: slower. 704.8 us (+244.0%).
